# Kernel optimization log

Measured on AMD Instinct MI355X. Metric: run time of the kernel, lower is better.

The kernel has to match this reference:

```python
import jax, jax.numpy as jnp
import numpy as np

B = 4096        # batch (number of bags)
L = 64          # num_lookups per bag
NT = 4          # number of embedding tables
V = 500000      # rows per table
D = 128         # emb_dim
DENSE = 512     # dense feature dim
BOT = [512, 1024, 512, 128]
TOP = [D * (1 + NT), 1024, 512, 1]  # [640, 1024, 512, 1]


def _linear_params(key, dims):
    params = []
    for i in range(len(dims) - 1):
        din, dout = dims[i], dims[i + 1]
        kw, kb, key = jax.random.split(key, 3)
        sw = np.sqrt(2.0 / (din + dout)).astype(np.float32)
        sb = np.sqrt(1.0 / dout).astype(np.float32)
        params.append((sw * jax.random.normal(kw, (dout, din), jnp.float32),
                       sb * jax.random.normal(kb, (dout,), jnp.float32)))
    return params


def setup_inputs() -> dict:
    key = jax.random.key(0)
    k_dense, k_idx, k_tab, k_bot, k_top = jax.random.split(key, 5)
    inp = {}
    inp["x_dense"] = jax.random.normal(k_dense, (B, DENSE), jnp.float32)
    bound = float(np.sqrt(1.0 / V))
    inp["tables"] = jax.random.uniform(k_tab, (NT, V, D), jnp.float32, -bound, bound)
    bot = _linear_params(k_bot, BOT)
    top = _linear_params(k_top, TOP)
    inp["bw0"], inp["bb0"] = bot[0]
    inp["bw1"], inp["bb1"] = bot[1]
    inp["bw2"], inp["bb2"] = bot[2]
    inp["tw0"], inp["tb0"] = top[0]
    inp["tw1"], inp["tb1"] = top[1]
    inp["tw2"], inp["tb2"] = top[2]
    inp["x_indices"] = jax.random.randint(k_idx, (B * L, NT), 0, V, dtype=jnp.int32)
    inp["constant_offsets"] = jnp.arange(B, dtype=jnp.int32) * L  # offsets of each bag
    return inp


def reference(x_dense, tables, bw0, bb0, bw1, bb1, bw2, bb2,
              tw0, tb0, tw1, tb1, tw2, tb2, x_indices, constant_offsets):
    # bottom MLP: Linear+ReLU x3
    h = jax.nn.relu(x_dense @ bw0.T + bb0)
    h = jax.nn.relu(h @ bw1.T + bb1)
    bot_out = jax.nn.relu(h @ bw2.T + bb2)                     # [B, D]

    # EmbeddingBag (sum mode) per table, driven by offsets
    N = x_indices.shape[0]
    seg = jnp.searchsorted(constant_offsets, jnp.arange(N, dtype=constant_offsets.dtype),
                           side='right') - 1                    # [N] bag id per index
    gathered = jax.vmap(lambda tab, idx: tab[idx])(tables, x_indices.T)  # [NT, N, D]
    pooled = jax.vmap(lambda e: jax.ops.segment_sum(e, seg, num_segments=B))(gathered)  # [NT, B, D]

    # concat order: bottom MLP out, then tables 1..4 (columns 0..3)
    feat = jnp.concatenate([bot_out] + [pooled[t] for t in range(NT)], axis=1)  # [B, 640]

    # top MLP: ReLU, ReLU, Sigmoid
    z = jax.nn.relu(feat @ tw0.T + tb0)
    z = jax.nn.relu(z @ tw1.T + tb1)
    out = jax.nn.sigmoid(z @ tw2.T + tb2)                       # [B, 1]
    return out
```

## Files before the change

### kernel.cpp

```cpp
#include <hip/hip_runtime.h>
#include <hip/hip_bf16.h>
#include <cstdint>

#define B_BAGS 4096
#define L_LOOK 64
#define NT 4
#define V_ROWS 500000
#define D_EMB 128
#define FEAT 640

typedef _Float16 half8 __attribute__((ext_vector_type(8)));
typedef _Float16 half4 __attribute__((ext_vector_type(4)));
typedef float f32x4 __attribute__((ext_vector_type(4)));

#define GLOAD_LDS(g, l) __builtin_amdgcn_global_load_lds( \
    (const __attribute__((address_space(1))) void*)(g),   \
    (__attribute__((address_space(3))) void*)(l), 16, 0, 0)

struct CvtArgs {
    const float* src[7];
    _Float16*    dst[7];
    int          n4[7];
};

__global__ __launch_bounds__(256) void cvt_kernel(CvtArgs a) {
    const int stride = gridDim.x * blockDim.x;
    const int t0 = blockIdx.x * blockDim.x + threadIdx.x;
#pragma unroll
    for (int t = 0; t < 7; ++t) {
        const float4* s = (const float4*)a.src[t];
        half4* d = (half4*)a.dst[t];
        for (int i = t0; i < a.n4[t]; i += stride) {
            float4 v = s[i];
            half4 h = { (_Float16)v.x, (_Float16)v.y, (_Float16)v.z, (_Float16)v.w };
            d[i] = h;
        }
    }
}

template<int BM, int BN, bool RELU>
__device__ __forceinline__ void gemm_body(
    _Float16* lds,
    int bm, int bn,
    const _Float16* __restrict__ X, int ldx,
    const _Float16* __restrict__ W, int ldw,
    const float* __restrict__ bias,
    _Float16* __restrict__ Y, int ldy,
    int K)
{
    constexpr int BK = 64;
    constexpr int FM = BM / 32;
    constexpr int FN = BN / 32;
    constexpr int AI = BM * 8 / 256;
    constexpr int BI = BN * 8 / 256;

    _Float16* As = lds;
    _Float16* Bs = lds + BM * BK;

    const int tid  = threadIdx.x;
    const int lane = tid & 63;
    const int wave = tid >> 6;
    const int wm   = wave >> 1;
    const int wn   = wave & 1;
    const int q    = lane >> 4;
    const int r16  = lane & 15;

    f32x4 acc[FM][FN] = {};

    for (int k0 = 0; k0 < K; k0 += BK) {
#pragma unroll
        for (int i = 0; i < AI; ++i) {
            int L = i * 256 + tid;
            int row = L >> 3, sl = L & 7;
            const _Float16* src = X + (size_t)(bm + row) * ldx + k0 + ((sl ^ (row & 7)) * 8);
            GLOAD_LDS(src, As + (size_t)(i * 256 + wave * 64) * 8);
        }
#pragma unroll
        for (int j = 0; j < BI; ++j) {
            int L = j * 256 + tid;
            int row = L >> 3, sl = L & 7;
            const _Float16* src = W + (size_t)(bn + row) * ldw + k0 + ((sl ^ (row & 7)) * 8);
            GLOAD_LDS(src, Bs + (size_t)(j * 256 + wave * 64) * 8);
        }
        __syncthreads();

#pragma unroll
        for (int s = 0; s < 2; ++s) {
            half8 a[FM], b[FN];
#pragma unroll
            for (int i = 0; i < FM; ++i) {
                int R = wm * (BM / 2) + i * 16 + r16;
                int sl = (s * 4 + q) ^ (R & 7);
                a[i] = *(const half8*)(As + R * BK + sl * 8);
            }
#pragma unroll
            for (int j = 0; j < FN; ++j) {
                int R = wn * (BN / 2) + j * 16 + r16;
                int sl = (s * 4 + q) ^ (R & 7);
                b[j] = *(const half8*)(Bs + R * BK + sl * 8);
            }
#pragma unroll
            for (int i = 0; i < FM; ++i)
#pragma unroll
                for (int j = 0; j < FN; ++j)
                    acc[i][j] = __builtin_amdgcn_mfma_f32_16x16x32_f16(
                        a[i], b[j], acc[i][j], 0, 0, 0);
        }
        __syncthreads();
    }

#pragma unroll
    for (int i = 0; i < FM; ++i) {
        const int m0 = bm + wm * (BM / 2) + i * 16 + q * 4;
#pragma unroll
        for (int j = 0; j < FN; ++j) {
            const int n = bn + wn * (BN / 2) + j * 16 + r16;
            const float bv = bias[n];
#pragma unroll
            for (int e = 0; e < 4; ++e) {
                float o = acc[i][j][e] + bv;
                if (RELU) o = fmaxf(o, 0.f);
                Y[(size_t)(m0 + e) * ldy + n] = (_Float16)o;
            }
        }
    }
}

template<int BM, int BN, bool RELU>
__global__ __launch_bounds__(256) void gemm_h(
    const _Float16* __restrict__ X, int ldx,
    const _Float16* __restrict__ W, int ldw,
    const float* __restrict__ bias,
    _Float16* __restrict__ Y, int ldy,
    int K)
{
    __shared__ __align__(16) _Float16 lds[(BM + BN) * 64];
    gemm_body<BM, BN, RELU>(lds, blockIdx.y * BM, blockIdx.x * BN,
                            X, ldx, W, ldw, bias, Y, ldy, K);
}

__device__ __forceinline__ void emb_body(
    int bag,
    const float* __restrict__ tables,
    const int*   __restrict__ idx,
    _Float16*    __restrict__ feat)
{
    const int wave = threadIdx.x >> 6;
    const int lane = threadIdx.x & 63;
    const int l5   = lane >> 5;
    const int c    = lane & 31;

    const int my_idx = idx[((size_t)bag * L_LOOK + lane) * NT + wave];
    const float* tab = tables + (size_t)wave * V_ROWS * D_EMB;

    float4 acc = {0.f, 0.f, 0.f, 0.f};
#pragma unroll 16
    for (int j = 0; j < 32; ++j) {
        int r = __shfl(my_idx, 2 * j + l5, 64);
        float4 v = ((const float4*)(tab + (size_t)r * D_EMB))[c];
        acc.x += v.x; acc.y += v.y; acc.z += v.z; acc.w += v.w;
    }
    acc.x += __shfl_xor(acc.x, 32, 64);
    acc.y += __shfl_xor(acc.y, 32, 64);
    acc.z += __shfl_xor(acc.z, 32, 64);
    acc.w += __shfl_xor(acc.w, 32, 64);
    if (l5 == 0) {
        half4 h = { (_Float16)acc.x, (_Float16)acc.y, (_Float16)acc.z, (_Float16)acc.w };
        *(half4*)(feat + (size_t)bag * FEAT + D_EMB + wave * D_EMB + c * 4) = h;
    }
}

__global__ __launch_bounds__(256) void fused_emb_gemm1(
    const _Float16* __restrict__ xh, const _Float16* __restrict__ bw0h,
    const float* __restrict__ bb0, _Float16* __restrict__ h0h,
    const float* __restrict__ tables, const int* __restrict__ idx,
    _Float16* __restrict__ feat)
{
    __shared__ __align__(16) _Float16 lds[(64 + 128) * 64];
    const int bid = blockIdx.x;
    if (bid < 512) {
        const int bn = (bid >> 6) * 128;
        const int bm = (bid & 63) * 64;
        gemm_body<64, 128, true>(lds, bm, bn, xh, 512, bw0h, 512, bb0, h0h, 1024, 512);
    } else {
        emb_body(bid - 512, tables, idx, feat);
    }
}

__global__ __launch_bounds__(256) void top2_h(
    const _Float16* __restrict__ Z,
    const _Float16* __restrict__ w,
    const float* __restrict__ bsc,
    float* __restrict__ out)
{
    const int row  = blockIdx.x * 4 + (threadIdx.x >> 6);
    const int lane = threadIdx.x & 63;

    half8 z  = *(const half8*)(Z + (size_t)row * 512 + lane * 8);
    half8 wv = *(const half8*)(w + lane * 8);
    float s = 0.f;
#pragma unroll
    for (int i = 0; i < 8; ++i) s += (float)z[i] * (float)wv[i];
#pragma unroll
    for (int off = 32; off > 0; off >>= 1) s += __shfl_down(s, off, 64);
    if (lane == 0) {
        float x = s + bsc[0];
        out[row] = 1.f / (1.f + expf(-x));
    }
}

extern "C" void kernel_launch(void* const* d_in, const int* in_sizes, int n_in,
                              void* d_out, int out_size, void* d_ws, size_t ws_size,
                              hipStream_t stream) {
    const float* x_dense = (const float*)d_in[0];
    const float* tables  = (const float*)d_in[1];
    const float* bw0 = (const float*)d_in[2];
    const float* bb0 = (const float*)d_in[3];
    const float* bw1 = (const float*)d_in[4];
    const float* bb1 = (const float*)d_in[5];
    const float* bw2 = (const float*)d_in[6];
    const float* bb2 = (const float*)d_in[7];
    const float* tw0 = (const float*)d_in[8];
    const float* tb0 = (const float*)d_in[9];
    const float* tw1 = (const float*)d_in[10];
    const float* tb1 = (const float*)d_in[11];
    const float* tw2 = (const float*)d_in[12];
    const float* tb2 = (const float*)d_in[13];
    const int*   x_idx = (const int*)d_in[14];
    float* out = (float*)d_out;

    char* p = (char*)d_ws;
    auto alloc = [&](size_t bytes) {
        char* r = p; p += (bytes + 255) & ~(size_t)255; return r;
    };
    _Float16* xh   = (_Float16*)alloc((size_t)4096 * 512 * 2);
    _Float16* bw0h = (_Float16*)alloc((size_t)1024 * 512 * 2);
    _Float16* bw1h = (_Float16*)alloc((size_t)512 * 1024 * 2);
    _Float16* bw2h = (_Float16*)alloc((size_t)128 * 512 * 2);
    _Float16* tw0h = (_Float16*)alloc((size_t)1024 * 640 * 2);
    _Float16* tw1h = (_Float16*)alloc((size_t)512 * 1024 * 2);
    _Float16* tw2h = (_Float16*)alloc((size_t)512 * 2);
    _Float16* h0h  = (_Float16*)alloc((size_t)4096 * 1024 * 2);
    _Float16* h1h  = (_Float16*)alloc((size_t)4096 * 512 * 2);
    _Float16* feat = (_Float16*)alloc((size_t)4096 * 640 * 2);
    _Float16* z0h  = (_Float16*)alloc((size_t)4096 * 1024 * 2);
    _Float16* z1h  = (_Float16*)alloc((size_t)4096 * 512 * 2);

    CvtArgs ca;
    ca.src[0] = x_dense; ca.dst[0] = xh;   ca.n4[0] = 4096 * 512 / 4;
    ca.src[1] = bw0;     ca.dst[1] = bw0h; ca.n4[1] = 1024 * 512 / 4;
    ca.src[2] = bw1;     ca.dst[2] = bw1h; ca.n4[2] = 512 * 1024 / 4;
    ca.src[3] = bw2;     ca.dst[3] = bw2h; ca.n4[3] = 128 * 512 / 4;
    ca.src[4] = tw0;     ca.dst[4] = tw0h; ca.n4[4] = 1024 * 640 / 4;
    ca.src[5] = tw1;     ca.dst[5] = tw1h; ca.n4[5] = 512 * 1024 / 4;
    ca.src[6] = tw2;     ca.dst[6] = tw2h; ca.n4[6] = 512 / 4;

    dim3 blk(256);

    cvt_kernel<<<dim3(1024), blk, 0, stream>>>(ca);

    fused_emb_gemm1<<<dim3(512 + B_BAGS), blk, 0, stream>>>(
        xh, bw0h, bb0, h0h, tables, x_idx, feat);

    gemm_h<64, 128, true><<<dim3(4, 64), blk, 0, stream>>>(
        h0h, 1024, bw1h, 1024, bb1, h1h, 512, 1024);

    gemm_h<64, 128, true><<<dim3(1, 64), blk, 0, stream>>>(
        h1h, 512, bw2h, 512, bb2, feat, 640, 512);

    gemm_h<64, 128, true><<<dim3(8, 64), blk, 0, stream>>>(
        feat, 640, tw0h, 640, tb0, z0h, 1024, 640);

    gemm_h<64, 128, true><<<dim3(4, 64), blk, 0, stream>>>(
        z0h, 1024, tw1h, 1024, tb1, z1h, 512, 1024);

    top2_h<<<dim3(1024), blk, 0, stream>>>(z1h, tw2h, tb2, out);
}
```

Measured before the change: 173.2 us.

## Spread embedding-bag and weight conversion across bottom-MLP GEMM launches

```diff
diff --git a/kernel.cpp b/kernel.cpp
--- a/kernel.cpp
+++ b/kernel.cpp
@@ -16,27 +16,6 @@
 #define GLOAD_LDS(g, l) __builtin_amdgcn_global_load_lds( \
     (const __attribute__((address_space(1))) void*)(g),   \
     (__attribute__((address_space(3))) void*)(l), 16, 0, 0)
-
-struct CvtArgs {
-    const float* src[7];
-    _Float16*    dst[7];
-    int          n4[7];
-};
-
-__global__ __launch_bounds__(256) void cvt_kernel(CvtArgs a) {
-    const int stride = gridDim.x * blockDim.x;
-    const int t0 = blockIdx.x * blockDim.x + threadIdx.x;
-#pragma unroll
-    for (int t = 0; t < 7; ++t) {
-        const float4* s = (const float4*)a.src[t];
-        half4* d = (half4*)a.dst[t];
-        for (int i = t0; i < a.n4[t]; i += stride) {
-            float4 v = s[i];
-            half4 h = { (_Float16)v.x, (_Float16)v.y, (_Float16)v.z, (_Float16)v.w };
-            d[i] = h;
-        }
-    }
-}
 
 template<int BM, int BN, bool RELU>
 __device__ __forceinline__ void gemm_body(
@@ -127,7 +106,7 @@
 }
 
 template<int BM, int BN, bool RELU>
-__global__ __launch_bounds__(256) void gemm_h(
+__global__ __launch_bounds__(256, 3) void gemm_h(
     const _Float16* __restrict__ X, int ldx,
     const _Float16* __restrict__ W, int ldw,
     const float* __restrict__ bias,
@@ -170,20 +149,64 @@
     }
 }
 
-__global__ __launch_bounds__(256) void fused_emb_gemm1(
-    const _Float16* __restrict__ xh, const _Float16* __restrict__ bw0h,
-    const float* __restrict__ bb0, _Float16* __restrict__ h0h,
-    const float* __restrict__ tables, const int* __restrict__ idx,
-    _Float16* __restrict__ feat)
-{
-    __shared__ __align__(16) _Float16 lds[(64 + 128) * 64];
+struct CvtRest {
+    const float* src[5];
+    _Float16*    dst[5];
+    int          n4[5];
+};
+
+template<int BM, int BN, bool RELU>
+__global__ __launch_bounds__(256, 3) void fused_gemm_emb(
+    const _Float16* __restrict__ X, int ldx,
+    const _Float16* __restrict__ W, int ldw,
+    const float* __restrict__ bias,
+    _Float16* __restrict__ Y, int ldy, int K,
+    int gemmBlocks, int mTiles,
+    int cvtBlocks, CvtRest cvt,
+    int embBase,
+    const float* __restrict__ tables,
+    const int*   __restrict__ idx,
+    _Float16*    __restrict__ feat)
+{
+    __shared__ __align__(16) _Float16 lds[(BM + BN) * 64];
     const int bid = blockIdx.x;
-    if (bid < 512) {
-        const int bn = (bid >> 6) * 128;
-        const int bm = (bid & 63) * 64;
-        gemm_body<64, 128, true>(lds, bm, bn, xh, 512, bw0h, 512, bb0, h0h, 1024, 512);
+    if (bid < gemmBlocks) {
+        const int bm = (bid % mTiles) * BM;
+        const int bn = (bid / mTiles) * BN;
+        gemm_body<BM, BN, RELU>(lds, bm, bn, X, ldx, W, ldw, bias, Y, ldy, K);
+    } else if (bid < gemmBlocks + cvtBlocks) {
+        const int t0 = (bid - gemmBlocks) * 256 + threadIdx.x;
+        const int stride = cvtBlocks * 256;
+#pragma unroll
+        for (int t = 0; t < 5; ++t) {
+            const float4* s = (const float4*)cvt.src[t];
+            half4* d = (half4*)cvt.dst[t];
+            for (int i = t0; i < cvt.n4[t]; i += stride) {
+                float4 v = s[i];
+                half4 h = { (_Float16)v.x, (_Float16)v.y, (_Float16)v.z, (_Float16)v.w };
+                d[i] = h;
+            }
+        }
     } else {
-        emb_body(bid - 512, tables, idx, feat);
+        emb_body(embBase + (bid - gemmBlocks - cvtBlocks), tables, idx, feat);
+    }
+}
+
+__global__ __launch_bounds__(256) void cvt2_kernel(
+    const float* __restrict__ s0, _Float16* __restrict__ d0, int n0,
+    const float* __restrict__ s1, _Float16* __restrict__ d1, int n1)
+{
+    const int stride = gridDim.x * blockDim.x;
+    const int t0 = blockIdx.x * blockDim.x + threadIdx.x;
+    for (int i = t0; i < n0; i += stride) {
+        float4 v = ((const float4*)s0)[i];
+        half4 h = { (_Float16)v.x, (_Float16)v.y, (_Float16)v.z, (_Float16)v.w };
+        ((half4*)d0)[i] = h;
+    }
+    for (int i = t0; i < n1; i += stride) {
+        float4 v = ((const float4*)s1)[i];
+        half4 h = { (_Float16)v.x, (_Float16)v.y, (_Float16)v.z, (_Float16)v.w };
+        ((half4*)d1)[i] = h;
     }
 }
 
@@ -246,32 +269,37 @@
     _Float16* z0h  = (_Float16*)alloc((size_t)4096 * 1024 * 2);
     _Float16* z1h  = (_Float16*)alloc((size_t)4096 * 512 * 2);
 
-    CvtArgs ca;
-    ca.src[0] = x_dense; ca.dst[0] = xh;   ca.n4[0] = 4096 * 512 / 4;
-    ca.src[1] = bw0;     ca.dst[1] = bw0h; ca.n4[1] = 1024 * 512 / 4;
-    ca.src[2] = bw1;     ca.dst[2] = bw1h; ca.n4[2] = 512 * 1024 / 4;
-    ca.src[3] = bw2;     ca.dst[3] = bw2h; ca.n4[3] = 128 * 512 / 4;
-    ca.src[4] = tw0;     ca.dst[4] = tw0h; ca.n4[4] = 1024 * 640 / 4;
-    ca.src[5] = tw1;     ca.dst[5] = tw1h; ca.n4[5] = 512 * 1024 / 4;
-    ca.src[6] = tw2;     ca.dst[6] = tw2h; ca.n4[6] = 512 / 4;
+    CvtRest cr;
+    cr.src[0] = bw1; cr.dst[0] = bw1h; cr.n4[0] = 512 * 1024 / 4;
+    cr.src[1] = bw2; cr.dst[1] = bw2h; cr.n4[1] = 128 * 512 / 4;
+    cr.src[2] = tw0; cr.dst[2] = tw0h; cr.n4[2] = 1024 * 640 / 4;
+    cr.src[3] = tw1; cr.dst[3] = tw1h; cr.n4[3] = 512 * 1024 / 4;
+    cr.src[4] = tw2; cr.dst[4] = tw2h; cr.n4[4] = 512 / 4;
+
+    CvtRest cr0 = {};
+    for (int i = 0; i < 5; ++i) { cr0.src[i] = bw1; cr0.dst[i] = bw1h; cr0.n4[i] = 0; }
 
     dim3 blk(256);
 
-    cvt_kernel<<<dim3(1024), blk, 0, stream>>>(ca);
-
-    fused_emb_gemm1<<<dim3(512 + B_BAGS), blk, 0, stream>>>(
-        xh, bw0h, bb0, h0h, tables, x_idx, feat);
-
-    gemm_h<64, 128, true><<<dim3(4, 64), blk, 0, stream>>>(
-        h0h, 1024, bw1h, 1024, bb1, h1h, 512, 1024);
-
-    gemm_h<64, 128, true><<<dim3(1, 64), blk, 0, stream>>>(
-        h1h, 512, bw2h, 512, bb2, feat, 640, 512);
-
-    gemm_h<64, 128, true><<<dim3(8, 64), blk, 0, stream>>>(
+    cvt2_kernel<<<dim3(128), blk, 0, stream>>>(
+        x_dense, xh, 4096 * 512 / 4, bw0, bw0h, 1024 * 512 / 4);
+
+    fused_gemm_emb<128, 128, true><<<dim3(256 + 64 + 2048), blk, 0, stream>>>(
+        xh, 512, bw0h, 512, bb0, h0h, 1024, 512,
+        256, 32, 64, cr, 0, tables, x_idx, feat);
+
+    fused_gemm_emb<128, 128, true><<<dim3(128 + 1280), blk, 0, stream>>>(
+        h0h, 1024, bw1h, 1024, bb1, h1h, 512, 1024,
+        128, 32, 0, cr0, 2048, tables, x_idx, feat);
+
+    fused_gemm_emb<128, 128, true><<<dim3(32 + 768), blk, 0, stream>>>(
+        h1h, 512, bw2h, 512, bb2, feat, 640, 512,
+        32, 32, 0, cr0, 3328, tables, x_idx, feat);
+
+    gemm_h<128, 128, true><<<dim3(8, 32), blk, 0, stream>>>(
         feat, 640, tw0h, 640, tb0, z0h, 1024, 640);
 
-    gemm_h<64, 128, true><<<dim3(4, 64), blk, 0, stream>>>(
+    gemm_h<128, 128, true><<<dim3(4, 32), blk, 0, stream>>>(
         z0h, 1024, tw1h, 1024, tb1, z1h, 512, 1024);
 
     top2_h<<<dim3(1024), blk, 0, stream>>>(z1h, tw2h, tb2, out);
```

New measurement: 166.7 us. 3.7% less time.
